# Kernel tuning notes

Hardware: AMD Instinct MI355X
Metric: run time of the kernel (lower is better)

## Reference

```python
import jax, jax.numpy as jnp
import numpy as np

B, L, HID = 512, 128, 384
N_LABELS, N_SLOTS = 32, 128


def setup_inputs() -> dict:
    key = jax.random.key(0)
    ks = jax.random.split(key, 16)

    def g(k, shape, scale):
        return jax.random.normal(k, shape, dtype=jnp.float32) * scale

    sent_lens = jax.random.randint(ks[0], (B,), 1, L + 1)
    mask = (jnp.arange(L)[None, :] < sent_lens[:, None]).astype(jnp.float32)[..., None]
    # zero out padded token positions to mimic the ragged original
    H = g(ks[1], (B, L, HID), 1.0) * mask
    c_slot_cont = g(ks[2], (B, L, HID), 1.0) * mask
    c_inte = g(ks[3], (B, HID), 1.0)
    s = 1.0 / np.sqrt(HID)
    return {
        "H": H,
        "c_slot_cont": c_slot_cont,
        "c_inte": c_inte,
        "W0": g(ks[4], (HID, HID), s),
        "W1": g(ks[5], (HID, HID), s),
        "W2": g(ks[6], (HID, HID), s),
        "W3": g(ks[7], (HID, HID), s),
        "W4": g(ks[8], (HID, HID), s),
        "b4": g(ks[9], (HID,), s),
        "W5": g(ks[10], (HID, 1), s),
        "V_SF": g(ks[11], (HID, HID), s),
        "W_inte": g(ks[12], (HID, N_LABELS), s),
        "W_slot": g(ks[13], (2 * HID, N_SLOTS), s),
        "sent_lens": sent_lens,
        "iteration_num": 3,
    }


def reference(H, c_slot_cont, c_inte, W0, W1, W2, W3, W4, b4, W5, V_SF,
              W_inte, W_slot, sent_lens, iteration_num):
    Ld = H.shape[1]
    mask = jnp.arange(Ld)[None, :] < sent_lens[:, None]          # [B, L] bool
    maskf = mask[..., None].astype(H.dtype)                       # [B, L, 1]
    neg_inf = jnp.finfo(H.dtype).min

    def sf_fusion(x, y):
        # SF_FusionLayer (dropout off / eval); inner loop runs once since nth=2
        x0 = jnp.tanh(x)
        y0 = jnp.tanh(y)
        f = jax.nn.sigmoid(jnp.tanh(x0 @ W0 + y0 @ W1) @ W2)
        x2 = f * x0 + x
        y2 = (1.0 - f) * y0 + y
        return f * x2 + (1.0 - f) * y2

    def id_fusion(x, y):
        # ID_FusionLayer; softmax over token dim, masked per sentence
        x0 = jnp.tanh(x)
        y0 = jnp.tanh(y)
        rates = ((x @ W3 + y @ W4 + b4) @ W5)[..., 0]             # [B, L]
        rates = jnp.where(mask, rates, neg_inf)
        alphas = jax.nn.softmax(rates, axis=1)[..., None]         # [B, L, 1]
        x2 = alphas * x0 + x
        y2 = (1.0 - alphas) * y0 + y
        return alphas * x2 + (1.0 - alphas) * y2

    r_inte = c_inte                                               # [B, HID]
    r_slot = c_slot_cont
    for _ in range(iteration_num):
        f_slot = sf_fusion(c_slot_cont, r_inte[:, None, :])       # [B, L, HID]
        f_slot = jnp.sum((f_slot @ V_SF) * maskf, axis=1)         # [B, HID]
        r_slot = f_slot[:, None, :] * c_slot_cont                 # [B, L, HID]
        f_inte = jnp.sum(id_fusion(r_slot, H) * maskf, axis=1)    # [B, HID]
        r_inte = f_inte + c_inte

    intent_output = r_inte @ W_inte                               # [B, n_labels]
    slot_output = jnp.concatenate([H, r_slot], axis=-1) @ W_slot  # [B, L, n_slots]
    return intent_output, slot_output
```

## Files before the change

### kernel.cpp

```cpp
#include <hip/hip_runtime.h>
#include <math.h>

#define HID 384
#define SLEN 128
#define NB 512
#define MTOK (NB*SLEN)
#define NLAB 32
#define NSLOT 128
#define APITCH 40
#define GPITCH 72

typedef _Float16 h8 __attribute__((ext_vector_type(8)));
typedef _Float16 h4v __attribute__((ext_vector_type(4)));
typedef __bf16   b8 __attribute__((ext_vector_type(8)));
typedef float    f4 __attribute__((ext_vector_type(4)));

__device__ __forceinline__ float sane(float x){
  return __builtin_isfinite(x) ? x : 0.f;
}
__device__ __forceinline__ float clampf(float x, float lo, float hi){
  return fminf(hi, fmaxf(lo, x));
}
__device__ __forceinline__ float fast_rcp(float x){
  return __builtin_amdgcn_rcpf(x);
}
__device__ __forceinline__ float fast_tanh(float x){
  x = clampf(x, -15.f, 15.f);
  float e = __expf(2.f * x);
  return (e - 1.f) * fast_rcp(e + 1.f);
}
__device__ __forceinline__ float sigmoid_c(float x){
  x = clampf(x, -60.f, 60.f);
  return fast_rcp(1.f + __expf(-x));
}
__device__ __forceinline__ void split16(float x, _Float16* h, _Float16* l){
  _Float16 hh = (_Float16)x; *h = hh; *l = (_Float16)(x - (float)hh);
}
__device__ __forceinline__ h8 ldh(const _Float16* p){ return *reinterpret_cast<const h8*>(p); }
__device__ __forceinline__ b8 ldb(const __bf16* p){ return *reinterpret_cast<const b8*>(p); }
__device__ __forceinline__ f4 mfma16h(h8 a, h8 b, f4 c){
  return __builtin_amdgcn_mfma_f32_16x16x32_f16(a, b, c, 0, 0, 0);
}
__device__ __forceinline__ f4 mfma16b(b8 a, b8 b, f4 c){
  return __builtin_amdgcn_mfma_f32_16x16x32_bf16(a, b, c, 0, 0, 0);
}


__global__ void k_lens(const int* __restrict__ raw, int* __restrict__ lensN){
  const int b = threadIdx.x;
  __shared__ int is64;
  if (b == 0) is64 = (raw[1] == 0) ? 1 : 0;
  __syncthreads();
  int v = is64 ? raw[2 * b] : raw[b];
  v = v < 0 ? 0 : (v > SLEN ? SLEN : v);
  lensN[b] = v;
}

__global__ void k_wsplit16(const float* __restrict__ in, _Float16* __restrict__ outh,
                           _Float16* __restrict__ outl, int R, int C){
  int idx = blockIdx.x * blockDim.x + threadIdx.x;
  if (idx < R * C){
    int r = idx / C, c = idx - r * C;
    float v = sane(in[idx]);
    _Float16 h = (_Float16)v;
    outh[(size_t)c * R + r] = h;
    outl[(size_t)c * R + r] = (_Float16)(v - (float)h);
  }
}

__global__ void k_wsplitbf(const float* __restrict__ in, __bf16* __restrict__ outh,
                           __bf16* __restrict__ outl, int R, int C){
  int idx = blockIdx.x * blockDim.x + threadIdx.x;
  if (idx < R * C){
    int r = idx / C, c = idx - r * C;
    float v = sane(in[idx]);
    __bf16 h = (__bf16)v;
    outh[(size_t)c * R + r] = h;
    outl[(size_t)c * R + r] = (__bf16)(v - (float)h);
  }
}

__global__ void k_transpose32(const float* __restrict__ in, float* __restrict__ out,
                              int R, int C){
  int idx = blockIdx.x * blockDim.x + threadIdx.x;
  if (idx < R * C){ int r = idx / C, c = idx - r * C; out[(size_t)c * R + r] = sane(in[idx]); }
}

__global__ void k_sanecopy(const float* __restrict__ in, float* __restrict__ out, int n){
  int i = blockIdx.x * blockDim.x + threadIdx.x;
  if (i < n) out[i] = sane(in[i]);
}

__global__ void k_w35(const float* __restrict__ W3, const float* __restrict__ W4,
                      const float* __restrict__ b4, const float* __restrict__ W5,
                      float* __restrict__ w35, float* __restrict__ w45, float* __restrict__ b45){
  __shared__ float w5s[HID];
  int t = threadIdx.x;
  w5s[t] = sane(W5[t]);
  __syncthreads();
  float s3 = 0.f, s4 = 0.f;
  for (int j = 0; j < HID; ++j){
    float w5 = w5s[j];
    s3 += sane(W3[(size_t)t * HID + j]) * w5;
    s4 += sane(W4[(size_t)t * HID + j]) * w5;
  }
  w35[t] = s3; w45[t] = s4;
  if (t == 0){
    float s = 0.f;
    for (int j = 0; j < HID; ++j) s += sane(b4[j]) * w5s[j];
    *b45 = s;
  }
}

__global__ void k_ci(const float* __restrict__ ci, float* __restrict__ r_inte){
  size_t i = blockIdx.x * (size_t)blockDim.x + threadIdx.x;
  if (i < (size_t)NB * HID) r_inte[i] = sane(ci[i]);
}

__global__ void k_hy(const float* __restrict__ Hm, const float* __restrict__ w45,
                     const float* __restrict__ b45, float* __restrict__ hy){
  int wave = threadIdx.x >> 6, lane = threadIdx.x & 63;
  int tok = blockIdx.x * 4 + wave;
  const float* row = Hm + (size_t)tok * HID;
  float s = 0.f;
#pragma unroll
  for (int i = 0; i < 6; ++i){ int k = lane + 64 * i; s += sane(row[k]) * w45[k]; }
  for (int off = 32; off; off >>= 1) s += __shfl_down(s, off);
  if (lane == 0) hy[tok] = clampf(s + *b45, -1e30f, 1e30f);
}

template <int TANH>
__global__ void k_vecmat(const float* __restrict__ in, const float* __restrict__ W,
                         float* __restrict__ out, float* __restrict__ pre_store){
  const int b = blockIdx.x, t = threadIdx.x;
  __shared__ float v[HID];
  float x = in[(size_t)b * HID + t];
  if (TANH) x = fast_tanh(x);
  v[t] = x;
  if (pre_store) pre_store[(size_t)b * HID + t] = x;
  __syncthreads();
  float s = 0.f;
  for (int k = 0; k < HID; ++k) s += v[k] * W[(size_t)k * HID + t];
  out[(size_t)b * HID + t] = clampf(s, -1e30f, 1e30f);
}

__global__ void __launch_bounds__(256, 3) k_p0c(
    const float* __restrict__ Cs,
    const _Float16* __restrict__ Wth, const _Float16* __restrict__ Wtl,
    const int* __restrict__ lens,
    _Float16* __restrict__ P0h, _Float16* __restrict__ P0l){
  __shared__ _Float16 Ah[128*APITCH], Al[128*APITCH], Bh[128*APITCH], Bl[128*APITCH];
  const int t = threadIdx.x;
  const int wave = t >> 6, lane = t & 63, quad = lane >> 4, lr = lane & 15;
  const int wm = wave & 1, wn = wave >> 1;
  const int bx = blockIdx.x, by = blockIdx.y;
  const int len = lens[bx];
  const bool live = (wm * 64) < len;
  f4 acc[4][4] = {};
  for (int kk = 0; kk < HID; kk += 32){
#pragma unroll
    for (int i = 0; i < 4; ++i){
      const int tau = t + 256 * i;
      const int row = tau >> 3, f4i = tau & 7;
      f4 v = *(const f4*)(Cs + ((size_t)(bx * 128 + row)) * HID + kk + f4i * 4);
      h4v hh, ll;
#pragma unroll
      for (int j = 0; j < 4; ++j){
        float x = fast_tanh(sane(v[j]));
        _Float16 h = (_Float16)x;
        hh[j] = h; ll[j] = (_Float16)(x - (float)h);
      }
      *(h4v*)&Ah[row * APITCH + f4i * 4] = hh;
      *(h4v*)&Al[row * APITCH + f4i * 4] = ll;
    }
#pragma unroll
    for (int i = 0; i < 4; ++i){
      const int tau = t + 256 * i;
      const int plane = tau >> 9;
      const int row = (tau >> 2) & 127;
      const int v8 = (tau & 3) << 3;
      const size_t gb = ((size_t)(by * 128 + row)) * HID + kk + v8;
      if (plane == 0) *(h8*)&Bh[row * APITCH + v8] = ldh(Wth + gb);
      else            *(h8*)&Bl[row * APITCH + v8] = ldh(Wtl + gb);
    }
    __syncthreads();
    if (live){
      h8 ah[4], al[4];
#pragma unroll
      for (int mi = 0; mi < 4; ++mi){
        int r = (wm * 64 + mi * 16 + lr) * APITCH + quad * 8;
        ah[mi] = *(h8*)&Ah[r]; al[mi] = *(h8*)&Al[r];
      }
#pragma unroll
      for (int ni = 0; ni < 4; ++ni){
        int r = (wn * 64 + ni * 16 + lr) * APITCH + quad * 8;
        h8 bh = *(h8*)&Bh[r], bl = *(h8*)&Bl[r];
#pragma unroll
        for (int mi = 0; mi < 4; ++mi){
          acc[mi][ni] = mfma16h(ah[mi], bh, acc[mi][ni]);
          acc[mi][ni] = mfma16h(ah[mi], bl, acc[mi][ni]);
          acc[mi][ni] = mfma16h(al[mi], bh, acc[mi][ni]);
        }
      }
    }
    __syncthreads();
  }
  if (live){
#pragma unroll
    for (int ni = 0; ni < 4; ++ni){
      int col = by * 128 + wn * 64 + ni * 16 + lr;
#pragma unroll
      for (int mi = 0; mi < 4; ++mi)
#pragma unroll
        for (int r = 0; r < 4; ++r){
          int rl = wm * 64 + mi * 16 + quad * 4 + r;
          if (rl < len){
            size_t o = ((size_t)(bx * 128 + rl)) * HID + col;
            _Float16 h, l; split16(acc[mi][ni][r], &h, &l);
            P0h[o] = h; P0l[o] = l;
          }
        }
    }
  }
}

__global__ void __launch_bounds__(512, 4) k_g2n(
    const _Float16* __restrict__ P0h, const _Float16* __restrict__ P0l,
    const _Float16* __restrict__ Wth, const _Float16* __restrict__ Wtl,
    const float* __restrict__ yw1, const float* __restrict__ Cs,
    const float* __restrict__ r_inte,
    const int* __restrict__ lens, float* __restrict__ S){
  __shared__ _Float16 Ah[64*GPITCH], Al[64*GPITCH];
  __shared__ float ywS[HID];
  const int t = threadIdx.x;
  const int wave = t >> 6, lane = t & 63, quad = lane >> 4, lr = lane & 15;
  const int bx = blockIdx.x;
  const int b = bx >> 1;
  const int len = lens[b];
  const int row0 = (bx & 1) * 64;
  if (row0 >= len) return;
  const int gr0 = bx * 64;
  const int srow = t >> 3;
  const int sk8 = (t & 7) << 3;
  const int col0 = wave * 48;
  if (t < HID) ywS[t] = yw1[(size_t)b * HID + t];
  __syncthreads();
  f4 acc[4][3] = {};
  for (int ks = 0; ks < 6; ++ks){
    const int kk = ks * 64;
    {
      const size_t g = ((size_t)(gr0 + srow)) * HID + kk + sk8;
      h8 ph = ldh(P0h + g), pl = ldh(P0l + g);
      const f4 ywa = *(const f4*)&ywS[kk + sk8];
      const f4 ywb = *(const f4*)&ywS[kk + sk8 + 4];
      h8 th, tl;
#pragma unroll
      for (int j = 0; j < 8; ++j){
        const float yw = (j < 4) ? ywa[j] : ywb[j - 4];
        float x = fast_tanh((float)ph[j] + (float)pl[j] + yw);
        _Float16 h = (_Float16)x;
        th[j] = h; tl[j] = (_Float16)(x - (float)h);
      }
      *(h8*)&Ah[srow * GPITCH + sk8] = th;
      *(h8*)&Al[srow * GPITCH + sk8] = tl;
    }
    __syncthreads();
#pragma unroll
    for (int c = 0; c < 2; ++c){
      const int ro = c * 32 + quad * 8;
      h8 amh[4], aml[4];
#pragma unroll
      for (int mi = 0; mi < 4; ++mi){
        const int r = (mi * 16 + lr) * GPITCH + ro;
        amh[mi] = *(const h8*)&Ah[r]; aml[mi] = *(const h8*)&Al[r];
      }
#pragma unroll
      for (int ni = 0; ni < 3; ++ni){
        const size_t rb = ((size_t)(col0 + ni * 16 + lr)) * HID + kk + ro;
        h8 bh = ldh(Wth + rb), bl = ldh(Wtl + rb);
#pragma unroll
        for (int mi = 0; mi < 4; ++mi){
          acc[mi][ni] = mfma16h(amh[mi], bh, acc[mi][ni]);
          acc[mi][ni] = mfma16h(amh[mi], bl, acc[mi][ni]);
          acc[mi][ni] = mfma16h(aml[mi], bh, acc[mi][ni]);
        }
      }
    }
    __syncthreads();
  }
  const float* rb = r_inte + (size_t)b * HID;
#pragma unroll
  for (int ni = 0; ni < 3; ++ni){
    const int col = col0 + ni * 16 + lr;
    const float yv = rb[col];
    const float y0 = fast_tanh(yv);
    float csum = 0.f;
#pragma unroll
    for (int mi = 0; mi < 4; ++mi)
#pragma unroll
      for (int r = 0; r < 4; ++r){
        const int rl = row0 + mi * 16 + quad * 4 + r;
        const int grow = gr0 + mi * 16 + quad * 4 + r;
        const float f = sigmoid_c(acc[mi][ni][r]);
        const float omf = 1.f - f;
        const float xv = sane(Cs[(size_t)grow * HID + col]);
        const float x0 = fast_tanh(xv);
        const float outv = f * f * x0 + f * xv + omf * omf * y0 + omf * yv;
        csum += (rl < len) ? outv : 0.f;
      }
    csum += __shfl_xor(csum, 16);
    csum += __shfl_xor(csum, 32);
    if (quad == 0) atomicAdd(&S[(size_t)b * HID + col], csum);
  }
}

__global__ void k_stageD2(
    const float* __restrict__ Cs, const float* __restrict__ Hm,
    const float* __restrict__ ci, const float* __restrict__ Vsc,
    const float* __restrict__ W1c, const float* __restrict__ w35,
    const float* __restrict__ hy, const int* __restrict__ lens,
    float* __restrict__ S, float* __restrict__ fss_g,
    float* __restrict__ r_inte, float* __restrict__ yw1){
  const int b = blockIdx.x;
  const int t = threadIdx.x;
  const int len = lens[b];
  __shared__ float Sl[HID], fssS[HID], fssw[HID], tri[HID];
  __shared__ float rates[SLEN];
  __shared__ float wA[SLEN], wB[SLEN], wC[SLEN], wD[SLEN];
  Sl[t] = S[(size_t)b * HID + t];
  S[(size_t)b * HID + t] = 0.f;
  __syncthreads();
  {
    float s = 0.f;
    for (int k = 0; k < HID; ++k) s += Sl[k] * Vsc[(size_t)k * HID + t];
    const float fs = clampf(s, -1e30f, 1e30f);
    fssS[t] = fs; fssw[t] = fs * w35[t];
    fss_g[(size_t)b * HID + t] = fs;
  }
  __syncthreads();
  const int wave = t >> 6, lane = t & 63;
  for (int l = wave; l < SLEN; l += 6){
    const float* row = Cs + ((size_t)b * SLEN + l) * HID;
    float s = 0.f;
#pragma unroll
    for (int i = 0; i < 6; ++i){ int k = lane + 64 * i; s += sane(row[k]) * fssw[k]; }
    for (int off = 32; off; off >>= 1) s += __shfl_down(s, off);
    if (lane == 0) rates[l] = clampf(s + hy[(size_t)b * SLEN + l], -1e30f, 1e30f);
  }
  __syncthreads();
  if (wave == 0){
    float r0 = (lane < len) ? rates[lane] : -3.0e38f;
    float r1 = (lane + 64 < len) ? rates[lane + 64] : -3.0e38f;
    float mx = fmaxf(r0, r1);
    for (int off = 32; off; off >>= 1) mx = fmaxf(mx, __shfl_xor(mx, off));
    float e0 = (lane < len) ? __expf(r0 - mx) : 0.f;
    float e1 = (lane + 64 < len) ? __expf(r1 - mx) : 0.f;
    float sm = e0 + e1;
    for (int off = 32; off; off >>= 1) sm += __shfl_xor(sm, off);
    const float inv = (sm > 0.f) ? (1.f / sm) : 0.f;
    float a0 = clampf(e0 * inv, 0.f, 1.f), a1 = clampf(e1 * inv, 0.f, 1.f);
    wA[lane] = a0 * a0; wB[lane] = a0;
    wC[lane] = (1.f - a0) * (1.f - a0); wD[lane] = 1.f - a0;
    wA[lane + 64] = a1 * a1; wB[lane + 64] = a1;
    wC[lane + 64] = (1.f - a1) * (1.f - a1); wD[lane + 64] = 1.f - a1;
  }
  __syncthreads();
  {
    const float fs = fssS[t];
    float acc = 0.f;
#pragma unroll 4
    for (int l = 0; l < len; ++l){
      const float cv = sane(Cs[((size_t)b * SLEN + l) * HID + t]);
      const float hv = sane(Hm[((size_t)b * SLEN + l) * HID + t]);
      const float rs = fs * cv;
      acc += wA[l] * fast_tanh(rs) + wB[l] * rs + wC[l] * fast_tanh(hv) + wD[l] * hv;
    }
    const float ri = clampf(acc + sane(ci[(size_t)b * HID + t]), -1e30f, 1e30f);
    r_inte[(size_t)b * HID + t] = ri;
    tri[t] = fast_tanh(ri);
  }
  __syncthreads();
  {
    float s = 0.f;
    for (int k = 0; k < HID; ++k) s += tri[k] * W1c[(size_t)k * HID + t];
    yw1[(size_t)b * HID + t] = clampf(s, -1e30f, 1e30f);
  }
}

__global__ void k_intent(const float* __restrict__ r_inte, const float* __restrict__ Wit,
                         float* __restrict__ out){
  const int t = threadIdx.x;
  const int b = blockIdx.x * 4 + (t >> 5);
  const int n = t & 31;
  const float* wr = Wit + (size_t)n * HID;
  const float* rr = r_inte + (size_t)b * HID;
  float s = 0.f;
  for (int k = 0; k < HID; ++k) s += rr[k] * wr[k];
  out[(size_t)b * NLAB + n] = clampf(s, -3e38f, 3e38f);
}

__global__ void __launch_bounds__(256, 2) k_slot_bf(
    const float* __restrict__ Hm, const float* __restrict__ Cs,
    const float* __restrict__ fss, const int* __restrict__ lens,
    const __bf16* __restrict__ Wth, const __bf16* __restrict__ Wtl,
    float* __restrict__ out){
  const int wave = threadIdx.x >> 6, lane = threadIdx.x & 63;
  const int quad = lane >> 4, lr = lane & 15;
  const int m0 = blockIdx.x * 128 + (wave & 1) * 64;
  const int n0 = (wave >> 1) * 64;
  const int b = blockIdx.x;
  const int ko = quad * 8;
  const int len = lens[b];
  if ((wave & 1) * 64 >= len){
#pragma unroll
    for (int mi = 0; mi < 4; ++mi)
#pragma unroll
      for (int ni = 0; ni < 4; ++ni)
#pragma unroll
        for (int r = 0; r < 4; ++r){
          const int row = m0 + mi * 16 + quad * 4 + r;
          const int col = n0 + ni * 16 + lr;
          out[(size_t)row * NSLOT + col] = 0.f;
        }
    return;
  }
  f4 acc[4][4] = {};
  for (int kk = 0; kk < 2 * HID; kk += 32){
    b8 ah[4], al[4], bh[4], bl[4];
#pragma unroll
    for (int i = 0; i < 4; ++i){
      size_t rb = (size_t)(n0 + i * 16 + lr) * (2 * HID) + kk + ko;
      bh[i] = ldb(Wth + rb); bl[i] = ldb(Wtl + rb);
    }
    if (kk < HID){
#pragma unroll
      for (int i = 0; i < 4; ++i){
        const float* hrow = Hm + (size_t)(m0 + i * 16 + lr) * HID + kk + ko;
        b8 vh, vl;
#pragma unroll
        for (int j = 0; j < 8; ++j){
          float v = sane(hrow[j]);
          __bf16 h = (__bf16)v;
          vh[j] = h; vl[j] = (__bf16)(v - (float)h);
        }
        ah[i] = vh; al[i] = vl;
      }
    } else {
      const int k2 = kk - HID + ko;
      float fv[8];
#pragma unroll
      for (int j = 0; j < 8; ++j) fv[j] = fss[(size_t)b * HID + k2 + j];
#pragma unroll
      for (int i = 0; i < 4; ++i){
        const float* crow = Cs + (size_t)(m0 + i * 16 + lr) * HID + k2;
        b8 vh, vl;
#pragma unroll
        for (int j = 0; j < 8; ++j){
          float v = fv[j] * sane(crow[j]);
          __bf16 h = (__bf16)v;
          vh[j] = h; vl[j] = (__bf16)(v - (float)h);
        }
        ah[i] = vh; al[i] = vl;
      }
    }
#pragma unroll
    for (int mi = 0; mi < 4; ++mi)
#pragma unroll
      for (int ni = 0; ni < 4; ++ni){
        acc[mi][ni] = mfma16b(ah[mi], bh[ni], acc[mi][ni]);
        acc[mi][ni] = mfma16b(ah[mi], bl[ni], acc[mi][ni]);
        acc[mi][ni] = mfma16b(al[mi], bh[ni], acc[mi][ni]);
      }
  }
#pragma unroll
  for (int mi = 0; mi < 4; ++mi)
#pragma unroll
    for (int ni = 0; ni < 4; ++ni)
#pragma unroll
      for (int r = 0; r < 4; ++r){
        const int row = m0 + mi * 16 + quad * 4 + r;
        const int col = n0 + ni * 16 + lr;
        out[(size_t)row * NSLOT + col] = clampf(acc[mi][ni][r], -3e38f, 3e38f);
      }
}

extern "C" void kernel_launch(void* const* d_in, const int* in_sizes, int n_in,
                              void* d_out, int out_size, void* d_ws, size_t ws_size,
                              hipStream_t stream){
  (void)in_sizes; (void)n_in; (void)out_size;
  const float* Hm  = (const float*)d_in[0];
  const float* Cs  = (const float*)d_in[1];
  const float* ci  = (const float*)d_in[2];
  const float* W0  = (const float*)d_in[3];
  const float* W1  = (const float*)d_in[4];
  const float* W2  = (const float*)d_in[5];
  const float* W3  = (const float*)d_in[6];
  const float* W4  = (const float*)d_in[7];
  const float* b4  = (const float*)d_in[8];
  const float* W5  = (const float*)d_in[9];
  const float* Vs  = (const float*)d_in[10];
  const float* Wi  = (const float*)d_in[11];
  const float* Wsl = (const float*)d_in[12];
  const int* lens_raw = (const int*)d_in[13];

  char* base = (char*)d_ws;
  size_t off = 0;
  auto alloc = [&](size_t bytes) -> void* {
    void* p = base + off; off += (bytes + 255) & ~(size_t)255; return p;
  };
  const size_t NT = (size_t)MTOK * HID;
  _Float16* P0h  = (_Float16*)alloc(NT * 2);
  _Float16* P0l  = (_Float16*)alloc(NT * 2);
  _Float16* W0th = (_Float16*)alloc((size_t)HID * HID * 2);
  _Float16* W0tl = (_Float16*)alloc((size_t)HID * HID * 2);
  _Float16* W2th = (_Float16*)alloc((size_t)HID * HID * 2);
  _Float16* W2tl = (_Float16*)alloc((size_t)HID * HID * 2);
  __bf16*   Wsth = (__bf16*)alloc((size_t)2 * HID * NSLOT * 2);
  __bf16*   Wstl = (__bf16*)alloc((size_t)2 * HID * NSLOT * 2);
  float* W1c    = (float*)alloc((size_t)HID * HID * 4);
  float* Vsc    = (float*)alloc((size_t)HID * HID * 4);
  float* Wit    = (float*)alloc((size_t)HID * NLAB * 4);
  float* w35    = (float*)alloc(HID * 4);
  float* w45    = (float*)alloc(HID * 4);
  float* b45    = (float*)alloc(4);
  float* hy     = (float*)alloc((size_t)MTOK * 4);
  float* yw1    = (float*)alloc((size_t)NB * HID * 4);
  float* r_inte = (float*)alloc((size_t)NB * HID * 4);
  float* S      = (float*)alloc((size_t)NB * HID * 4);
  float* fss    = (float*)alloc((size_t)NB * HID * 4);
  int* lensN    = (int*)alloc((size_t)NB * 4);
  if (off > ws_size) return;

  k_lens<<<1, NB, 0, stream>>>(lens_raw, lensN);
  k_wsplit16<<<(HID * HID + 255) / 256, 256, 0, stream>>>(W0, W0th, W0tl, HID, HID);
  k_wsplit16<<<(HID * HID + 255) / 256, 256, 0, stream>>>(W2, W2th, W2tl, HID, HID);
  k_wsplitbf<<<(2 * HID * NSLOT + 255) / 256, 256, 0, stream>>>(Wsl, Wsth, Wstl, 2 * HID, NSLOT);
  k_sanecopy<<<(HID * HID + 255) / 256, 256, 0, stream>>>(W1, W1c, HID * HID);
  k_sanecopy<<<(HID * HID + 255) / 256, 256, 0, stream>>>(Vs, Vsc, HID * HID);
  k_transpose32<<<(HID * NLAB + 255) / 256, 256, 0, stream>>>(Wi, Wit, HID, NLAB);
  k_w35<<<1, HID, 0, stream>>>(W3, W4, b4, W5, w35, w45, b45);
  k_ci<<<(NB * HID + 255) / 256, 256, 0, stream>>>(ci, r_inte);
  k_hy<<<MTOK / 4, 256, 0, stream>>>(Hm, w45, b45, hy);
  k_p0c<<<dim3(NB, 3), 256, 0, stream>>>(Cs, W0th, W0tl, lensN, P0h, P0l);

  k_vecmat<1><<<NB, HID, 0, stream>>>(r_inte, W1c, yw1, (float*)nullptr);
  hipMemsetAsync(S, 0, (size_t)NB * HID * 4, stream);

  for (int it = 0; it < 3; ++it){
    k_g2n<<<MTOK / 64, 512, 0, stream>>>(P0h, P0l, W2th, W2tl, yw1, Cs, r_inte, lensN, S);
    k_stageD2<<<NB, HID, 0, stream>>>(Cs, Hm, ci, Vsc, W1c, w35, hy, lensN,
                                      S, fss, r_inte, yw1);
  }

  float* outp = (float*)d_out;
  k_intent<<<NB / 4, 128, 0, stream>>>(r_inte, Wit, outp);
  k_slot_bf<<<NB, 256, 0, stream>>>(Hm, Cs, fss, lensN, Wsth, Wstl, outp + (size_t)NB * NLAB);
}
```

Before: 1.079 ms.

## Restructure P0 GEMM to g2n-style tiling with register prefetch and light barriers

Rewrites the tanh(C)@W0 GEMM kernel to match the g2n layout: 64-row tiles with 512 threads, each wave covering 48 output columns across the full width. B operands are read straight from global memory instead of being staged in LDS. Rows past the sentence length are now skipped per 64-row block rather than per wave. Both GEMM kernels prefetch the next K-slice of activations into registers before the barrier, and use a barrier that waits only on LDS counters instead of __syncthreads, so the global prefetch can stay in flight across it. The cost is more global and L2 traffic for W, since it is no longer shared through LDS within a block.

```diff
diff --git a/kernel.cpp b/kernel.cpp
--- a/kernel.cpp
+++ b/kernel.cpp
@@ -7,7 +7,6 @@
 #define MTOK (NB*SLEN)
 #define NLAB 32
 #define NSLOT 128
-#define APITCH 40
 #define GPITCH 72
 
 typedef _Float16 h8 __attribute__((ext_vector_type(8)));
@@ -43,6 +42,10 @@
 }
 __device__ __forceinline__ f4 mfma16b(b8 a, b8 b, f4 c){
   return __builtin_amdgcn_mfma_f32_16x16x32_bf16(a, b, c, 0, 0, 0);
+}
+__device__ __forceinline__ void bar_lds(){
+  asm volatile("s_waitcnt lgkmcnt(0)" ::: "memory");
+  __builtin_amdgcn_s_barrier();
 }
 
 
@@ -144,83 +147,82 @@
   out[(size_t)b * HID + t] = clampf(s, -1e30f, 1e30f);
 }
 
-__global__ void __launch_bounds__(256, 3) k_p0c(
+__global__ void __launch_bounds__(512, 4) k_p0c(
     const float* __restrict__ Cs,
     const _Float16* __restrict__ Wth, const _Float16* __restrict__ Wtl,
     const int* __restrict__ lens,
     _Float16* __restrict__ P0h, _Float16* __restrict__ P0l){
-  __shared__ _Float16 Ah[128*APITCH], Al[128*APITCH], Bh[128*APITCH], Bl[128*APITCH];
+  __shared__ _Float16 Ah[64*GPITCH], Al[64*GPITCH];
   const int t = threadIdx.x;
   const int wave = t >> 6, lane = t & 63, quad = lane >> 4, lr = lane & 15;
-  const int wm = wave & 1, wn = wave >> 1;
-  const int bx = blockIdx.x, by = blockIdx.y;
-  const int len = lens[bx];
-  const bool live = (wm * 64) < len;
-  f4 acc[4][4] = {};
-  for (int kk = 0; kk < HID; kk += 32){
-#pragma unroll
-    for (int i = 0; i < 4; ++i){
-      const int tau = t + 256 * i;
-      const int row = tau >> 3, f4i = tau & 7;
-      f4 v = *(const f4*)(Cs + ((size_t)(bx * 128 + row)) * HID + kk + f4i * 4);
-      h4v hh, ll;
-#pragma unroll
-      for (int j = 0; j < 4; ++j){
-        float x = fast_tanh(sane(v[j]));
+  const int bx = blockIdx.x;
+  const int b = bx >> 1;
+  const int len = lens[b];
+  const int row0 = (bx & 1) * 64;
+  if (row0 >= len) return;
+  const int gr0 = bx * 64;
+  const int srow = t >> 3;
+  const int sk8 = (t & 7) << 3;
+  const int col0 = wave * 48;
+  const float* abase = Cs + (size_t)(gr0 + srow) * HID + sk8;
+  f4 c0 = *(const f4*)(abase);
+  f4 c1 = *(const f4*)(abase + 4);
+  f4 acc[4][3] = {};
+  for (int ks = 0; ks < 6; ++ks){
+    const int kk = ks * 64;
+    {
+      h8 th, tl;
+#pragma unroll
+      for (int j = 0; j < 8; ++j){
+        float x = fast_tanh(sane((j < 4) ? c0[j] : c1[j - 4]));
         _Float16 h = (_Float16)x;
-        hh[j] = h; ll[j] = (_Float16)(x - (float)h);
-      }
-      *(h4v*)&Ah[row * APITCH + f4i * 4] = hh;
-      *(h4v*)&Al[row * APITCH + f4i * 4] = ll;
-    }
-#pragma unroll
-    for (int i = 0; i < 4; ++i){
-      const int tau = t + 256 * i;
-      const int plane = tau >> 9;
-      const int row = (tau >> 2) & 127;
-      const int v8 = (tau & 3) << 3;
-      const size_t gb = ((size_t)(by * 128 + row)) * HID + kk + v8;
-      if (plane == 0) *(h8*)&Bh[row * APITCH + v8] = ldh(Wth + gb);
-      else            *(h8*)&Bl[row * APITCH + v8] = ldh(Wtl + gb);
-    }
-    __syncthreads();
-    if (live){
-      h8 ah[4], al[4];
+        th[j] = h; tl[j] = (_Float16)(x - (float)h);
+      }
+      *(h8*)&Ah[srow * GPITCH + sk8] = th;
+      *(h8*)&Al[srow * GPITCH + sk8] = tl;
+    }
+    if (ks < 5){
+      c0 = *(const f4*)(abase + kk + 64);
+      c1 = *(const f4*)(abase + kk + 68);
+    }
+    bar_lds();
+#pragma unroll
+    for (int c = 0; c < 2; ++c){
+      const int ro = c * 32 + quad * 8;
+      h8 amh[4], aml[4];
 #pragma unroll
       for (int mi = 0; mi < 4; ++mi){
-        int r = (wm * 64 + mi * 16 + lr) * APITCH + quad * 8;
-        ah[mi] = *(h8*)&Ah[r]; al[mi] = *(h8*)&Al[r];
-      }
-#pragma unroll
-      for (int ni = 0; ni < 4; ++ni){
-        int r = (wn * 64 + ni * 16 + lr) * APITCH + quad * 8;
-        h8 bh = *(h8*)&Bh[r], bl = *(h8*)&Bl[r];
+        const int r = (mi * 16 + lr) * GPITCH + ro;
+        amh[mi] = *(const h8*)&Ah[r]; aml[mi] = *(const h8*)&Al[r];
+      }
+#pragma unroll
+      for (int ni = 0; ni < 3; ++ni){
+        const size_t rb = ((size_t)(col0 + ni * 16 + lr)) * HID + kk + ro;
+        h8 bh = ldh(Wth + rb), bl = ldh(Wtl + rb);
 #pragma unroll
         for (int mi = 0; mi < 4; ++mi){
-          acc[mi][ni] = mfma16h(ah[mi], bh, acc[mi][ni]);
-          acc[mi][ni] = mfma16h(ah[mi], bl, acc[mi][ni]);
-          acc[mi][ni] = mfma16h(al[mi], bh, acc[mi][ni]);
+          acc[mi][ni] = mfma16h(amh[mi], bh, acc[mi][ni]);
+          acc[mi][ni] = mfma16h(amh[mi], bl, acc[mi][ni]);
+          acc[mi][ni] = mfma16h(aml[mi], bh, acc[mi][ni]);
         }
       }
     }
-    __syncthreads();
-  }
-  if (live){
-#pragma unroll
-    for (int ni = 0; ni < 4; ++ni){
-      int col = by * 128 + wn * 64 + ni * 16 + lr;
-#pragma unroll
-      for (int mi = 0; mi < 4; ++mi)
-#pragma unroll
-        for (int r = 0; r < 4; ++r){
-          int rl = wm * 64 + mi * 16 + quad * 4 + r;
-          if (rl < len){
-            size_t o = ((size_t)(bx * 128 + rl)) * HID + col;
-            _Float16 h, l; split16(acc[mi][ni][r], &h, &l);
-            P0h[o] = h; P0l[o] = l;
-          }
+    bar_lds();
+  }
+#pragma unroll
+  for (int ni = 0; ni < 3; ++ni){
+    const int col = col0 + ni * 16 + lr;
+#pragma unroll
+    for (int mi = 0; mi < 4; ++mi)
+#pragma unroll
+      for (int r = 0; r < 4; ++r){
+        const int rl = row0 + mi * 16 + quad * 4 + r;
+        if (rl < len){
+          const size_t o = ((size_t)(b * SLEN + rl)) * HID + col;
+          _Float16 h, l; split16(acc[mi][ni][r], &h, &l);
+          P0h[o] = h; P0l[o] = l;
         }
-    }
+      }
   }
 }
 
@@ -245,12 +247,13 @@
   const int col0 = wave * 48;
   if (t < HID) ywS[t] = yw1[(size_t)b * HID + t];
   __syncthreads();
+  const _Float16* pbase = P0h + (size_t)(gr0 + srow) * HID + sk8;
+  const _Float16* lbase = P0l + (size_t)(gr0 + srow) * HID + sk8;
+  h8 ph = ldh(pbase), pl = ldh(lbase);
   f4 acc[4][3] = {};
   for (int ks = 0; ks < 6; ++ks){
     const int kk = ks * 64;
     {
-      const size_t g = ((size_t)(gr0 + srow)) * HID + kk + sk8;
-      h8 ph = ldh(P0h + g), pl = ldh(P0l + g);
       const f4 ywa = *(const f4*)&ywS[kk + sk8];
       const f4 ywb = *(const f4*)&ywS[kk + sk8 + 4];
       h8 th, tl;
@@ -264,7 +267,11 @@
       *(h8*)&Ah[srow * GPITCH + sk8] = th;
       *(h8*)&Al[srow * GPITCH + sk8] = tl;
     }
-    __syncthreads();
+    if (ks < 5){
+      ph = ldh(pbase + kk + 64);
+      pl = ldh(lbase + kk + 64);
+    }
+    bar_lds();
 #pragma unroll
     for (int c = 0; c < 2; ++c){
       const int ro = c * 32 + quad * 8;
@@ -286,7 +293,7 @@
         }
       }
     }
-    __syncthreads();
+    bar_lds();
   }
   const float* rb = r_inte + (size_t)b * HID;
 #pragma unroll
@@ -541,7 +548,7 @@
   k_w35<<<1, HID, 0, stream>>>(W3, W4, b4, W5, w35, w45, b45);
   k_ci<<<(NB * HID + 255) / 256, 256, 0, stream>>>(ci, r_inte);
   k_hy<<<MTOK / 4, 256, 0, stream>>>(Hm, w45, b45, hy);
-  k_p0c<<<dim3(NB, 3), 256, 0, stream>>>(Cs, W0th, W0tl, lensN, P0h, P0l);
+  k_p0c<<<MTOK / 64, 512, 0, stream>>>(Cs, W0th, W0tl, lensN, P0h, P0l);
 
   k_vecmat<1><<<NB, HID, 0, stream>>>(r_inte, W1c, yw1, (float*)nullptr);
   hipMemsetAsync(S, 0, (size_t)NB * HID * 4, stream);
```

Result: no change. 1.086 ms (+0.6%).
